# Optimization experiments

Hardware: AMD Instinct MI355X
Metric: run time of the kernel (lower is better)

## Reference

```python
import jax, jax.numpy as jnp
from jax import lax
import numpy as np

K = 10
N_SEEDS = 20


def farthest_point_sample(xyz, npoint):
    # xyz: [B, N, C] -> centroids [B, npoint] (int32)
    B, N, C = xyz.shape

    def step(carry, _):
        distance, farthest = carry
        centroid = jnp.take_along_axis(xyz, farthest[:, None, None], axis=1)  # [B,1,C]
        d = jnp.sum((xyz - centroid) ** 2, axis=-1)  # [B,N]
        distance = jnp.minimum(distance, d)
        new_farthest = jnp.argmax(distance, axis=-1)
        return (distance, new_farthest), farthest

    init = (jnp.full((B, N), 1e10, xyz.dtype), jnp.zeros((B,), jnp.int32))
    _, cents = lax.scan(step, init, None, length=npoint)  # [npoint, B]
    return cents.T  # [B, npoint]


def setup_inputs() -> dict:
    key = jax.random.key(0)
    pcs = jax.random.normal(key, (64, 16384, 3), dtype=jnp.float32)
    return {"pcs": pcs}


def reference(pcs):
    # pcs: [B, N, 3]
    seeds = farthest_point_sample(pcs, N_SEEDS)  # [B, n_seeds]
    seeds_value = jnp.take_along_axis(pcs, seeds[:, :, None], axis=1)  # [B, n_seeds, 3]
    # dist_new in the torch code: [B, n_seeds, N] (seed-to-point distances)
    diff = seeds_value[:, :, None, :] - pcs[:, None, :, :]  # [B, n_seeds, N, 3]
    dist_new = jnp.linalg.norm(diff, axis=-1)  # [B, n_seeds, N]
    # k+1 smallest distances per seed (ascending)
    neg_top, _ = lax.top_k(-dist_new, K + 1)
    top_dist = -neg_top  # [B, n_seeds, k+1], ascending
    overall_mean = jnp.mean(top_dist[:, :, 1:])
    top_dist = top_dist / overall_mean
    m = jnp.mean(top_dist, axis=2)  # [B, n_seeds]
    var = jnp.var(m, ddof=1)  # torch.var default: unbiased
    return var
```

## Files before the change

### kernel.cpp

```cpp
#include <hip/hip_runtime.h>

#pragma clang fp contract(off)

#define N_PTS   16384
#define N_SEEDS 20
#define KP1     11
#define NBIN    512
#define NREP    32
#define CAP     4096
#define NKNN    3

typedef unsigned long long u64;
typedef unsigned int       u32;

#define FMAXDPP(m, ctrl, rmask) { \
    const int _v = __builtin_amdgcn_update_dpp(__float_as_int(m), __float_as_int(m), \
                                               (ctrl), (rmask), 0xf, false); \
    m = fmaxf(m, __int_as_float(_v)); }

#define FDECL(i) float px##i, py##i, pz##i, dd##i = 1e10f;
#define LOADPTS(P4)                                                         \
    {   const int f4 = t * 12;                                              \
        const float4 q0 = P4[f4+0],  q1 = P4[f4+1],  q2  = P4[f4+2];        \
        const float4 q3 = P4[f4+3],  q4 = P4[f4+4],  q5  = P4[f4+5];        \
        const float4 q6 = P4[f4+6],  q7 = P4[f4+7],  q8  = P4[f4+8];        \
        const float4 q9 = P4[f4+9],  q10 = P4[f4+10], q11 = P4[f4+11];      \
        px0 =q0.x;  py0 =q0.y;  pz0 =q0.z;                                  \
        px1 =q0.w;  py1 =q1.x;  pz1 =q1.y;                                  \
        px2 =q1.z;  py2 =q1.w;  pz2 =q2.x;                                  \
        px3 =q2.y;  py3 =q2.z;  pz3 =q2.w;                                  \
        px4 =q3.x;  py4 =q3.y;  pz4 =q3.z;                                  \
        px5 =q3.w;  py5 =q4.x;  pz5 =q4.y;                                  \
        px6 =q4.z;  py6 =q4.w;  pz6 =q5.x;                                  \
        px7 =q5.y;  py7 =q5.z;  pz7 =q5.w;                                  \
        px8 =q6.x;  py8 =q6.y;  pz8 =q6.z;                                  \
        px9 =q6.w;  py9 =q7.x;  pz9 =q7.y;                                  \
        px10=q7.z;  py10=q7.w;  pz10=q8.x;                                  \
        px11=q8.y;  py11=q8.z;  pz11=q8.w;                                  \
        px12=q9.x;  py12=q9.y;  pz12=q9.z;                                  \
        px13=q9.w;  py13=q10.x; pz13=q10.y;                                 \
        px14=q10.z; py14=q10.w; pz14=q11.x;                                 \
        px15=q11.y; py15=q11.z; pz15=q11.w; }

__global__ __launch_bounds__(1024)
__attribute__((amdgpu_waves_per_eu(4, 4)))
void fused_kernel(const float* __restrict__ pcs,
                  int* __restrict__ seeds,
                  int* __restrict__ done,
                  float* __restrict__ topd,
                  float* __restrict__ out,
                  int B) {
    __shared__ alignas(16) u32 hist[NBIN * NREP];
    __shared__ u32    part[NBIN];
    __shared__ float  cand[CAP];
    __shared__ u32    cnt;
    __shared__ u32    s_thr;
    __shared__ int    s_sid;
    __shared__ float  s_val[2][16];
    __shared__ float4 s_pack[2][16];

    const int bid  = blockIdx.x;
    const int t    = threadIdx.x;
    const int lane = t & 63;
    const int wid  = t >> 6;

    if (bid < B) {
        const float* __restrict__ P  = pcs + (size_t)bid * N_PTS * 3;
        const float4* __restrict__ P4 = (const float4*)P;

        FDECL(0)  FDECL(1)  FDECL(2)  FDECL(3)
        FDECL(4)  FDECL(5)  FDECL(6)  FDECL(7)
        FDECL(8)  FDECL(9)  FDECL(10) FDECL(11)
        FDECL(12) FDECL(13) FDECL(14) FDECL(15)
        LOADPTS(P4)

        float cx = P[0], cy = P[1], cz = P[2];
        int farthest = 0;

        for (int it = 0; it < N_SEEDS; ++it) {
            if (t == 0)
                __hip_atomic_store(&seeds[bid * N_SEEDS + it], farthest,
                                   __ATOMIC_RELAXED, __HIP_MEMORY_SCOPE_AGENT);
            if (it == N_SEEDS - 1) break;

            float bestv = -1.0f, bx = 0.f, by = 0.f, bz = 0.f;
            int   besti = 0;
#define FSTEP(i) { const float dx = px##i - cx, dy = py##i - cy, dz = pz##i - cz; \
        const float d  = (dx*dx + dy*dy) + dz*dz; \
        const float nd = fminf(dd##i, d); dd##i = nd; \
        if (nd > bestv) { bestv = nd; besti = t*16 + (i); \
                          bx = px##i; by = py##i; bz = pz##i; } }
            FSTEP(0)  FSTEP(1)  FSTEP(2)  FSTEP(3)
            FSTEP(4)  FSTEP(5)  FSTEP(6)  FSTEP(7)
            FSTEP(8)  FSTEP(9)  FSTEP(10) FSTEP(11)
            FSTEP(12) FSTEP(13) FSTEP(14) FSTEP(15)

            float m = bestv;
            FMAXDPP(m, 0x111, 0xf)
            FMAXDPP(m, 0x112, 0xf)
            FMAXDPP(m, 0x114, 0xf)
            FMAXDPP(m, 0x118, 0xf)
            FMAXDPP(m, 0x142, 0xa)
            FMAXDPP(m, 0x143, 0xc)
            const float wmax = __int_as_float(
                __builtin_amdgcn_readlane(__float_as_int(m), 63));
            const u64 msk = __ballot(bestv == wmax);
            const int low = __ffsll((unsigned long long)msk) - 1;

            const int par = it & 1;
            if (lane == low) {
                s_val[par][wid]  = bestv;
                s_pack[par][wid] = make_float4(__int_as_float(besti), bx, by, bz);
            }
            __syncthreads();

            float v16 = s_val[par][lane & 15];
            float r = v16;
            FMAXDPP(r, 0x111, 0xf)
            FMAXDPP(r, 0x112, 0xf)
            FMAXDPP(r, 0x114, 0xf)
            FMAXDPP(r, 0x118, 0xf)
            const float gmax = __int_as_float(
                __builtin_amdgcn_readlane(__float_as_int(r), 15));
            const u64 m2 = __ballot(v16 == gmax) & 0xFFFFull;
            const int ws = __ffsll((unsigned long long)m2) - 1;
            const float4 pk = s_pack[par][ws];
            farthest = __float_as_int(pk.x);
            cx = pk.y; cy = pk.z; cz = pk.w;
        }
    } else {
        const int kk = bid - B;
        const int b  = kk % B;
        const int j  = kk / B;

        const float* __restrict__ P  = pcs + (size_t)b * N_PTS * 3;
        const float4* __restrict__ P4 = (const float4*)P;
        const int rep = t & 31;

        FDECL(0)  FDECL(1)  FDECL(2)  FDECL(3)
        FDECL(4)  FDECL(5)  FDECL(6)  FDECL(7)
        FDECL(8)  FDECL(9)  FDECL(10) FDECL(11)
        FDECL(12) FDECL(13) FDECL(14) FDECL(15)
        LOADPTS(P4)

#pragma unroll
        for (int i = 0; i < (NBIN * NREP) / 1024; ++i) hist[t + i * 1024] = 0u;
        if (t == 0) cnt = 0u;

        for (int s = j; s < N_SEEDS; s += NKNN) {
            if (t == 0) {
                int sv;
                while ((sv = __hip_atomic_load(&seeds[b * N_SEEDS + s],
                               __ATOMIC_RELAXED, __HIP_MEMORY_SCOPE_AGENT)) < 0)
                    __builtin_amdgcn_s_sleep(2);
                s_sid = sv;
            }
            __syncthreads();
            const int sid = s_sid;
            const float cx = P[sid*3], cy = P[sid*3+1], cz = P[sid*3+2];

#define HSTEP(i) { const float dx = px##i - cx, dy = py##i - cy, dz = pz##i - cz; \
        const float d = fmaf(dz, dz, fmaf(dy, dy, dx * dx)); \
        atomicAdd(&hist[(__float_as_uint(d) >> 22) * NREP + rep], 1u); }
            HSTEP(0)  HSTEP(1)  HSTEP(2)  HSTEP(3)
            HSTEP(4)  HSTEP(5)  HSTEP(6)  HSTEP(7)
            HSTEP(8)  HSTEP(9)  HSTEP(10) HSTEP(11)
            HSTEP(12) HSTEP(13) HSTEP(14) HSTEP(15)
            __syncthreads();

            if (t < NBIN) {
                u32 ssum = 0;
#pragma unroll
                for (int r2 = 0; r2 < NREP; ++r2)
                    ssum += hist[t * NREP + ((r2 + t) & (NREP - 1))];
                part[t] = ssum;
            }
            __syncthreads();

            if (wid == 0) {
                u32 s8 = 0;
#pragma unroll
                for (int i = 0; i < 8; ++i)
                    s8 += part[lane * 8 + ((i + lane) & 7)];
                u32 cum = s8;
                for (int off = 1; off < 64; off <<= 1) {
                    const u32 o = __shfl_up(cum, off);
                    if (lane >= off) cum += o;
                }
                const u64 mm = __ballot(cum >= (u32)KP1);
                const int L  = __ffsll((unsigned long long)mm) - 1;
                const u32 below = __shfl(cum - s8, L);
                const u32 bc = (lane < 8) ? part[L * 8 + lane] : 0u;
                u32 ic = bc;
                for (int off = 1; off < 8; off <<= 1) {
                    const u32 o = __shfl_up(ic, off);
                    if (lane >= off) ic += o;
                }
                const u64 mm2 = __ballot(lane < 8 && (below + ic) >= (u32)KP1);
                const int l2  = __ffsll((unsigned long long)mm2) - 1;
                if (lane == 0) s_thr = (u32)(L * 8 + l2 + 1) << 22;
            } else {
                if (t == 64) cnt = 0u;
                for (int i = t - 64; i < NBIN * NREP; i += 960) hist[i] = 0u;
            }
            __syncthreads();

            const float thrf = __uint_as_float(s_thr);
#define CSTEP(i) { const float dx = px##i - cx, dy = py##i - cy, dz = pz##i - cz; \
        const float d = fmaf(dz, dz, fmaf(dy, dy, dx * dx)); \
        if (d < thrf) { const u32 sl = atomicAdd(&cnt, 1u); \
                        if (sl < (u32)CAP) cand[sl] = d; } }
            CSTEP(0)  CSTEP(1)  CSTEP(2)  CSTEP(3)
            CSTEP(4)  CSTEP(5)  CSTEP(6)  CSTEP(7)
            CSTEP(8)  CSTEP(9)  CSTEP(10) CSTEP(11)
            CSTEP(12) CSTEP(13) CSTEP(14) CSTEP(15)
            __syncthreads();

            if (wid == 0) {
                const u32 n = min(cnt, (u32)CAP);
                for (u32 base = 0; base < n; base += 64) {
                    const u32 idx = base + (u32)lane;
                    const float vv = (idx < n) ? cand[idx] : 3.0e38f;
                    u32 r2 = 0;
                    for (u32 jj = 0; jj < n; ++jj) {
                        const float w = cand[jj];
                        r2 += (w < vv || (w == vv && jj < idx)) ? 1u : 0u;
                    }
                    if (idx < n && r2 < (u32)KP1)
                        topd[(b * N_SEEDS + s) * KP1 + r2] = sqrtf(vv);
                }
            }
        }

        __syncthreads();
        if (t == 0) {
            __threadfence();
            __hip_atomic_fetch_add(done, 1, __ATOMIC_RELAXED,
                                   __HIP_MEMORY_SCOPE_AGENT);
        }

        if (bid == B) {
            const int target = NKNN * B - 1;
            if (t == 0) {
                while (__hip_atomic_load(done, __ATOMIC_RELAXED,
                                         __HIP_MEMORY_SCOPE_AGENT) != target)
                    __builtin_amdgcn_s_sleep(8);
            }
            __syncthreads();
            __threadfence();

            const int pairs = B * N_SEEDS;
            const int total = pairs * KP1;
            double* red = (double*)hist;

            double s1 = 0.0;
            for (int i = t; i < total; i += 1024)
                if (i % KP1 != 0) s1 += (double)topd[i];
            red[t] = s1;
            __syncthreads();
            for (int off = 512; off; off >>= 1) {
                if (t < off) red[t] += red[t + off];
                __syncthreads();
            }
            const double om = red[0] / (double)(pairs * (KP1 - 1));

            double sm = 0.0, sm2 = 0.0;
            for (int pr = t; pr < pairs; pr += 1024) {
                double acc = 0.0;
                for (int jj = 0; jj < KP1; ++jj) acc += (double)topd[pr * KP1 + jj];
                const double m = acc / (om * (double)KP1);
                sm += m;
                sm2 += m * m;
            }
            __syncthreads();
            red[t] = sm;
            __syncthreads();
            for (int off = 512; off; off >>= 1) {
                if (t < off) red[t] += red[t + off];
                __syncthreads();
            }
            const double Sm = red[0];
            __syncthreads();
            red[t] = sm2;
            __syncthreads();
            for (int off = 512; off; off >>= 1) {
                if (t < off) red[t] += red[t + off];
                __syncthreads();
            }
            if (t == 0) {
                const double var = (red[0] - Sm * Sm / (double)pairs)
                                   / (double)(pairs - 1);
                out[0] = (float)var;
            }
        }
    }
}

extern "C" void kernel_launch(void* const* d_in, const int* in_sizes, int n_in,
                              void* d_out, int out_size, void* d_ws, size_t ws_size,
                              hipStream_t stream) {
    const float* pcs = (const float*)d_in[0];
    const int B = in_sizes[0] / (N_PTS * 3);

    int*   seeds = (int*)d_ws;
    int*   done  = (int*)((char*)d_ws + 5120);
    float* topd  = (float*)((char*)d_ws + 8192);
    float* out   = (float*)d_out;

    (void)hipMemsetAsync(d_ws, 0xFF, 8192, stream);

    fused_kernel<<<B * (1 + NKNN), 1024, 0, stream>>>(pcs, seeds, done, topd, out, B);
}
```

Before: 62.34 us.

## Accumulate per-pair stats with atomics and finalize in last-arriving block

Each kNN block now reduces its top-k distances with wave shuffles and adds three double sums (sum excluding self, total sum, squared total) to global accumulators. The finalizer block that spun on a counter and re-read all stored distances is replaced by a last-block-done pattern that computes the variance from these three sums. This drops the spin-wait and the serial final reduction tail. The cost is global double atomics, an extra memset, and a different summation order.

```diff
diff --git a/kernel.cpp b/kernel.cpp
--- a/kernel.cpp
+++ b/kernel.cpp
@@ -12,6 +12,20 @@
 
 typedef unsigned long long u64;
 typedef unsigned int       u32;
+
+__device__ __forceinline__ u64 shfl_xor_u64(u64 v, int off) {
+    int lo = __shfl_xor((int)(u32)(v & 0xffffffffull), off);
+    int hi = __shfl_xor((int)(u32)(v >> 32), off);
+    return ((u64)(u32)hi << 32) | (u32)lo;
+}
+
+__device__ __forceinline__ double wsum_f64(double v) {
+    for (int off = 32; off; off >>= 1) {
+        const u64 b = shfl_xor_u64((u64)__double_as_longlong(v), off);
+        v += __longlong_as_double((long long)b);
+    }
+    return v;
+}
 
 #define FMAXDPP(m, ctrl, rmask) { \
     const int _v = __builtin_amdgcn_update_dpp(__float_as_int(m), __float_as_int(m), \
@@ -47,7 +61,7 @@
 void fused_kernel(const float* __restrict__ pcs,
                   int* __restrict__ seeds,
                   int* __restrict__ done,
-                  float* __restrict__ topd,
+                  double* __restrict__ acc,
                   float* __restrict__ out,
                   int B) {
     __shared__ alignas(16) u32 hist[NBIN * NREP];
@@ -218,6 +232,7 @@
 
             if (wid == 0) {
                 const u32 n = min(cnt, (u32)CAP);
+                double psum = 0.0, self0 = 0.0;
                 for (u32 base = 0; base < n; base += 64) {
                     const u32 idx = base + (u32)lane;
                     const float vv = (idx < n) ? cand[idx] : 3.0e38f;
@@ -226,8 +241,18 @@
                         const float w = cand[jj];
                         r2 += (w < vv || (w == vv && jj < idx)) ? 1u : 0u;
                     }
-                    if (idx < n && r2 < (u32)KP1)
-                        topd[(b * N_SEEDS + s) * KP1 + r2] = sqrtf(vv);
+                    if (idx < n && r2 < (u32)KP1) {
+                        const double sv = (double)sqrtf(vv);
+                        psum += sv;
+                        if (r2 == 0u) self0 = sv;
+                    }
+                }
+                const double Ppair = wsum_f64(psum);
+                const double Spair = Ppair - wsum_f64(self0);
+                if (lane == 0) {
+                    atomicAdd(&acc[0], Spair);
+                    atomicAdd(&acc[1], Ppair);
+                    atomicAdd(&acc[2], Ppair * Ppair);
                 }
             }
         }
@@ -235,60 +260,17 @@
         __syncthreads();
         if (t == 0) {
             __threadfence();
-            __hip_atomic_fetch_add(done, 1, __ATOMIC_RELAXED,
-                                   __HIP_MEMORY_SCOPE_AGENT);
-        }
-
-        if (bid == B) {
-            const int target = NKNN * B - 1;
-            if (t == 0) {
-                while (__hip_atomic_load(done, __ATOMIC_RELAXED,
-                                         __HIP_MEMORY_SCOPE_AGENT) != target)
-                    __builtin_amdgcn_s_sleep(8);
-            }
-            __syncthreads();
-            __threadfence();
-
-            const int pairs = B * N_SEEDS;
-            const int total = pairs * KP1;
-            double* red = (double*)hist;
-
-            double s1 = 0.0;
-            for (int i = t; i < total; i += 1024)
-                if (i % KP1 != 0) s1 += (double)topd[i];
-            red[t] = s1;
-            __syncthreads();
-            for (int off = 512; off; off >>= 1) {
-                if (t < off) red[t] += red[t + off];
-                __syncthreads();
-            }
-            const double om = red[0] / (double)(pairs * (KP1 - 1));
-
-            double sm = 0.0, sm2 = 0.0;
-            for (int pr = t; pr < pairs; pr += 1024) {
-                double acc = 0.0;
-                for (int jj = 0; jj < KP1; ++jj) acc += (double)topd[pr * KP1 + jj];
-                const double m = acc / (om * (double)KP1);
-                sm += m;
-                sm2 += m * m;
-            }
-            __syncthreads();
-            red[t] = sm;
-            __syncthreads();
-            for (int off = 512; off; off >>= 1) {
-                if (t < off) red[t] += red[t + off];
-                __syncthreads();
-            }
-            const double Sm = red[0];
-            __syncthreads();
-            red[t] = sm2;
-            __syncthreads();
-            for (int off = 512; off; off >>= 1) {
-                if (t < off) red[t] += red[t + off];
-                __syncthreads();
-            }
-            if (t == 0) {
-                const double var = (red[0] - Sm * Sm / (double)pairs)
+            const int old = __hip_atomic_fetch_add(done, 1, __ATOMIC_RELAXED,
+                                                   __HIP_MEMORY_SCOPE_AGENT);
+            if (old == NKNN * B - 2) {
+                __threadfence();
+                const double S1 = acc[0], Pt = acc[1], Q = acc[2];
+                const int pairs = B * N_SEEDS;
+                const double om = S1 / (double)(pairs * (KP1 - 1));
+                const double d11 = om * (double)KP1;
+                const double sm = Pt / d11;
+                const double sq = Q / (d11 * d11);
+                const double var = (sq - sm * sm / (double)pairs)
                                    / (double)(pairs - 1);
                 out[0] = (float)var;
             }
@@ -302,12 +284,13 @@
     const float* pcs = (const float*)d_in[0];
     const int B = in_sizes[0] / (N_PTS * 3);
 
-    int*   seeds = (int*)d_ws;
-    int*   done  = (int*)((char*)d_ws + 5120);
-    float* topd  = (float*)((char*)d_ws + 8192);
-    float* out   = (float*)d_out;
+    int*    seeds = (int*)d_ws;
+    int*    done  = (int*)((char*)d_ws + 5120);
+    double* acc   = (double*)((char*)d_ws + 8192);
+    float*  out   = (float*)d_out;
 
     (void)hipMemsetAsync(d_ws, 0xFF, 8192, stream);
-
-    fused_kernel<<<B * (1 + NKNN), 1024, 0, stream>>>(pcs, seeds, done, topd, out, B);
-}
+    (void)hipMemsetAsync((char*)d_ws + 8192, 0x00, 64, stream);
+
+    fused_kernel<<<B * (1 + NKNN), 1024, 0, stream>>>(pcs, seeds, done, acc, out, B);
+}
```

Measured after the change: 71.86 us. +15.3%, slower.
